# Kernel optimization log

Hardware: AMD Instinct MI355X
Metric: run time of the kernel (lower is better)

Reference implementation:

```python
import jax, jax.numpy as jnp
import numpy as np

PATCH = 3
PAD = 1  # (patchsize-1)//2
PRETRAIN_DIM = 1024
TARGET_DIM = 1024
OUT_H, OUT_W = 224, 224


def _pool_matrix(L_in, L_out):
    """Matrix P s.t. x @ P == torch.adaptive_avg_pool1d(x, L_out)."""
    P = np.zeros((L_in, L_out), dtype=np.float32)
    for i in range(L_out):
        s = (i * L_in) // L_out
        e = -((-(i + 1) * L_in) // L_out)  # ceil
        P[s:e, i] = 1.0 / (e - s)
    return jnp.asarray(P)


def patchify(x):
    """[B,C,H,W] -> [B,H*W,C,3,3], matching Unfold(k=3,s=1,p=1) + reshape/permute."""
    B, C, H, W = x.shape
    xp = jnp.pad(x, ((0, 0), (0, 0), (PAD, PAD), (PAD, PAD)))
    # [B,C,3,3,H,W] with kernel offsets (ki,kj)
    cols = jnp.stack([
        jnp.stack([xp[:, :, i:i + H, j:j + W] for j in range(PATCH)], axis=3)
        for i in range(PATCH)], axis=2)
    return cols.transpose(0, 4, 5, 1, 2, 3).reshape(B, H * W, C, PATCH, PATCH)


def resize_bilinear(x, oh, ow):
    """Bilinear resize of last two dims, align_corners=False (torch semantics)."""
    H, W = x.shape[-2], x.shape[-1]

    def idx(L, O):
        src = (jnp.arange(O, dtype=jnp.float32) + 0.5) * (L / O) - 0.5
        src = jnp.clip(src, 0.0, L - 1)
        i0 = jnp.floor(src).astype(jnp.int32)
        i1 = jnp.minimum(i0 + 1, L - 1)
        return i0, i1, src - i0

    r0, r1, wr = idx(H, oh)
    c0, c1, wc = idx(W, ow)
    xr = x[..., r0, :] * (1.0 - wr)[:, None] + x[..., r1, :] * wr[:, None]
    return xr[..., c0] * (1.0 - wc) + xr[..., c1] * wc


def setup_inputs() -> dict:
    key = jax.random.key(0)
    k1, k2, k3 = jax.random.split(key, 3)
    return {
        "feat1": jax.random.normal(k1, (8, 512, 28, 28), dtype=jnp.float32),
        "feat2": jax.random.normal(k2, (8, 1024, 14, 14), dtype=jnp.float32),
        "memory": jax.random.normal(k3, (20000, 1024), dtype=jnp.float32),
    }


def reference(feat1, feat2, memory):
    B, C1, H1, W1 = feat1.shape
    _, C2, H2, W2 = feat2.shape
    N = H1 * W1  # reference patch grid

    # --- patchify (Unfold k=3 s=1 p=1) ---
    p1 = patchify(feat1)                      # [B, N, C1, 3, 3]
    p2 = patchify(feat2)                      # [B, H2*W2, C2, 3, 3]

    # --- multiscale bilinear resize of layer-2 patch grid to ref grid ---
    g = p2.reshape(B, H2, W2, C2, PATCH, PATCH).transpose(0, 3, 4, 5, 1, 2)  # [B,C2,3,3,H2,W2]
    g = resize_bilinear(g, H1, W1)                                           # [B,C2,3,3,H1,W1]
    p2 = g.transpose(0, 4, 5, 1, 2, 3).reshape(B, N, C2, PATCH, PATCH)

    # --- Preprocessing: adaptive_avg_pool1d over flattened patch -> pretrain dim ---
    f1 = p1.reshape(B * N, C1 * PATCH * PATCH) @ _pool_matrix(C1 * PATCH * PATCH, PRETRAIN_DIM)
    f2 = p2.reshape(B * N, C2 * PATCH * PATCH) @ _pool_matrix(C2 * PATCH * PATCH, PRETRAIN_DIM)

    # --- Aggregator: stack layers, adaptive pool to target dim ---
    stacked = jnp.stack([f1, f2], axis=1).reshape(B * N, 2 * PRETRAIN_DIM)
    feats = stacked @ _pool_matrix(2 * PRETRAIN_DIM, TARGET_DIM)  # [B*N, D]

    # --- kNN memory-bank scoring (k=1): min Euclidean distance ---
    d2 = (jnp.sum(feats * feats, axis=-1, keepdims=True)
          - 2.0 * feats @ memory.T
          + jnp.sum(memory * memory, axis=-1))  # [B*N, M]
    dist = jnp.sqrt(jnp.maximum(d2, 0.0))
    patch_scores = jnp.min(dist, axis=1)       # [B*N]

    # --- unpatch + score + raw segmentation map ---
    ps = patch_scores.reshape(B, N)
    image_scores = jnp.max(ps, axis=1)                           # [B]
    raw_maps = resize_bilinear(ps.reshape(B, H1, W1), OUT_H, OUT_W)  # [B,224,224]
    return image_scores, raw_maps
```

## Files before the change

kernel.cpp:

```cpp
#include <hip/hip_runtime.h>
#include <hip/hip_bf16.h>
#include <math.h>

#define BQ 8
#define C1N 512
#define N1 784
#define C2N 1024
#define M2 196
#define NROWS 6272
#define MEMN 20000
#define MEMNP 20096
#define DIMK 1024
#define NKB 32
#define KTB 4096
#define OUTHW 50176
#define NTILEA 49
#define NTILEB 157
#define NWG (NTILEB * NTILEA)

typedef unsigned char u8;
typedef long long i64v;

typedef __attribute__((ext_vector_type(4))) float f32x4;

static __device__ __forceinline__ unsigned int f2ord(float f) {
  unsigned int b = __float_as_uint(f);
  return (b & 0x80000000u) ? ~b : (b | 0x80000000u);
}
static __device__ __forceinline__ float ord2f(unsigned int u) {
  unsigned int b = (u & 0x80000000u) ? (u ^ 0x80000000u) : ~u;
  return __uint_as_float(b);
}

static __device__ __forceinline__ int pack4_fp8(float a, float b, float c, float d) {
  int lo = __builtin_amdgcn_cvt_pk_fp8_f32(a, b, 0, false);
  return __builtin_amdgcn_cvt_pk_fp8_f32(c, d, lo, true);
}
static __device__ __forceinline__ float sumsq4_fp8(int w) {
  float f0 = __builtin_amdgcn_cvt_f32_fp8(w, 0);
  float f1 = __builtin_amdgcn_cvt_f32_fp8(w, 1);
  float f2 = __builtin_amdgcn_cvt_f32_fp8(w, 2);
  float f3 = __builtin_amdgcn_cvt_f32_fp8(w, 3);
  return f0 * f0 + f1 * f1 + f2 * f2 + f3 * f3;
}

static __device__ __forceinline__ void gload16(const void* g, void* l) {
  __builtin_amdgcn_global_load_lds((const __attribute__((address_space(1))) void*)g,
                                   (__attribute__((address_space(3))) void*)l, 16, 0, 0);
}

static __device__ __forceinline__ size_t tiled_idx(int grow, int k) {
  int tile = grow >> 7, row = grow & 127;
  int kb = k >> 5, c = (k >> 3) & 3, e = k & 7;
  return (((size_t)(tile * NKB + kb) * 4 + c) * 128 + row) * 8 + e;
}

static __device__ __forceinline__ float f1val(const float* __restrict__ x, int b, unsigned L) {
  unsigned h = L % 28u; unsigned t = L / 28u;
  unsigned ki = t % 3u; t /= 3u;
  unsigned c = t % 512u; t /= 512u;
  unsigned w = t % 28u; unsigned kj = t / 28u;
  unsigned y = h + ki - 1u;
  unsigned xx = w + kj - 1u;
  if (y >= 28u || xx >= 28u) return 0.f;
  return x[(((size_t)b * 512u + c) * 28u + y) * 28u + xx];
}
static __device__ __forceinline__ float f2val(const float* __restrict__ x, int b, unsigned L) {
  unsigned h = L % 14u; unsigned t = L / 14u;
  unsigned ki = t % 3u; t /= 3u;
  unsigned c = t % 1024u; t /= 1024u;
  unsigned w = t % 14u; unsigned kj = t / 14u;
  unsigned y = h + ki - 1u;
  unsigned xx = w + kj - 1u;
  if (y >= 14u || xx >= 14u) return 0.f;
  return x[(((size_t)b * 1024u + c) * 14u + y) * 14u + xx];
}

__global__ __launch_bounds__(256) void feat_a_fp8(const float* __restrict__ feat1,
                                                  u8* __restrict__ At) {
  int id = blockIdx.x * 256 + threadIdx.x;
  if (id >= BQ * 64 * N1) return;
  int n = id % N1; int t = id / N1;
  int jc = t % 64; int b = t / 64;
  float v[8];
#pragma unroll
  for (int e = 0; e < 8; ++e) {
    int j = jc * 8 + e;
    unsigned L0 = 9u * (unsigned)(512 * n + j);
    float s = 0.f;
#pragma unroll
    for (int u = 0; u < 9; ++u) s += f1val(feat1, b, L0 + u);
    s += f1val(feat1, b, L0 + 4u);
    v[e] = s * 0.1f;
  }
  int w0 = pack4_fp8(v[0], v[1], v[2], v[3]);
  int w1 = pack4_fp8(v[4], v[5], v[6], v[7]);
  *(int2*)&At[tiled_idx(b * N1 + n, jc * 8)] = make_int2(w0, w1);
}

__global__ __launch_bounds__(256) void feat_b_stage1(const float* __restrict__ feat2,
                                                     float* __restrict__ H2all) {
  int b = blockIdx.x / M2;
  int n2 = blockIdx.x % M2;
  for (int i = threadIdx.x; i < 512; i += 256) {
    unsigned L0 = 18u * (unsigned)(512 * n2 + i);
    float s = 0.f;
#pragma unroll
    for (int u = 0; u < 18; ++u) s += f2val(feat2, b, L0 + u);
    H2all[((size_t)b * M2 + n2) * 512 + i] = s * (1.0f / 18.0f);
  }
}

__global__ __launch_bounds__(256) void feat_b_stage2_fp8(const float* __restrict__ H2all,
                                                         u8* __restrict__ At) {
  int id = blockIdx.x * 256 + threadIdx.x;
  if (id >= BQ * 64 * N1) return;
  int n = id % N1; int t = id / N1;
  int ic = t % 64; int b = t / 64;
  int y = n / 28, x = n % 28;
  float sy = 0.5f * (float)y - 0.25f;
  sy = fminf(fmaxf(sy, 0.f), 13.f);
  int y0 = (int)sy, y1 = min(y0 + 1, 13);
  float wy = sy - (float)y0;
  float sx = 0.5f * (float)x - 0.25f;
  sx = fminf(fmaxf(sx, 0.f), 13.f);
  int x0 = (int)sx, x1 = min(x0 + 1, 13);
  float wx = sx - (float)x0;
  float w00 = (1.f - wy) * (1.f - wx), w10 = wy * (1.f - wx);
  float w01 = (1.f - wy) * wx, w11 = wy * wx;
  const float* h00 = H2all + ((size_t)b * M2 + y0 * 14 + x0) * 512 + ic * 8;
  const float* h10 = H2all + ((size_t)b * M2 + y1 * 14 + x0) * 512 + ic * 8;
  const float* h01 = H2all + ((size_t)b * M2 + y0 * 14 + x1) * 512 + ic * 8;
  const float* h11 = H2all + ((size_t)b * M2 + y1 * 14 + x1) * 512 + ic * 8;
  float v[8];
#pragma unroll
  for (int e = 0; e < 8; ++e)
    v[e] = w00 * h00[e] + w10 * h10[e] + w01 * h01[e] + w11 * h11[e];
  int w0 = pack4_fp8(v[0], v[1], v[2], v[3]);
  int w1 = pack4_fp8(v[4], v[5], v[6], v[7]);
  *(int2*)&At[tiled_idx(b * N1 + n, 512 + ic * 8)] = make_int2(w0, w1);
}

__global__ __launch_bounds__(256) void memconv_fp8(const float* __restrict__ mem,
                                                   u8* __restrict__ Bt) {
  int gid = blockIdx.x * 256 + threadIdx.x;
  if (gid >= NTILEB * NKB * 512) return;
  int tile = gid >> 14;
  int within = gid & 16383;
  int kb = within >> 9;
  int u = within & 511;
  int c = u >> 7, row = u & 127;
  int n = tile * 128 + row;
  int k0 = kb * 32 + c * 8;
  int w0 = 0, w1 = 0;
  if (n < MEMN) {
    const float* src = mem + (size_t)n * DIMK + k0;
    float4 a = *(const float4*)src;
    float4 b = *(const float4*)(src + 4);
    w0 = pack4_fp8(a.x, a.y, a.z, a.w);
    w1 = pack4_fp8(b.x, b.y, b.z, b.w);
  }
  *(int2*)&Bt[(size_t)gid * 8] = make_int2(w0, w1);
}

__global__ __launch_bounds__(256) void fnorm_fp8(const u8* __restrict__ At,
                                                 float* __restrict__ fnorm) {
  int row = blockIdx.x * 4 + (threadIdx.x >> 6);
  int lane = threadIdx.x & 63;
  float s = 0.f;
#pragma unroll
  for (int qq = 0; qq < 2; ++qq) {
    int kc = lane * 2 + qq;
    int2 d = *(const int2*)&At[tiled_idx(row, kc * 8)];
    s += sumsq4_fp8(d.x);
    s += sumsq4_fp8(d.y);
  }
#pragma unroll
  for (int off = 32; off; off >>= 1) s += __shfl_down(s, off, 64);
  if (lane == 0) fnorm[row] = s;
}

__global__ __launch_bounds__(256) void mnorm_fp8(const float* __restrict__ memory,
                                                 float* __restrict__ mnorm) {
  __shared__ float red[4];
  const int row = blockIdx.x;
  const float4 v = *(const float4*)&memory[(size_t)row * DIMK + threadIdx.x * 4];
  int p0 = __builtin_amdgcn_cvt_pk_fp8_f32(v.x, v.y, 0, false);
  int p1 = __builtin_amdgcn_cvt_pk_fp8_f32(v.z, v.w, 0, false);
  float q0 = __builtin_amdgcn_cvt_f32_fp8(p0, 0);
  float q1 = __builtin_amdgcn_cvt_f32_fp8(p0, 1);
  float q2 = __builtin_amdgcn_cvt_f32_fp8(p1, 0);
  float q3 = __builtin_amdgcn_cvt_f32_fp8(p1, 1);
  float s = q0 * q0 + q1 * q1 + q2 * q2 + q3 * q3;
#pragma unroll
  for (int off = 32; off; off >>= 1) s += __shfl_down(s, off, 64);
  if ((threadIdx.x & 63) == 0) red[threadIdx.x >> 6] = s;
  __syncthreads();
  if (threadIdx.x == 0) mnorm[row] = red[0] + red[1] + red[2] + red[3];
}

__global__ __launch_bounds__(256, 4) void dist_min_mfma(const u8* __restrict__ At,
                                                        const u8* __restrict__ Bt,
                                                        const float* __restrict__ mnorm,
                                                        unsigned int* __restrict__ minu) {
  __shared__ __align__(16) u8 LAs[3][4096];
  __shared__ __align__(16) u8 LBs[3][4096];
  const int t = threadIdx.x;
  const int wave = t >> 6, lane = t & 63;

  int lid = blockIdx.x;
  const int q = NWG / 8, r = NWG % 8;
  int xcd = lid & 7, pos = lid >> 3;
  int wgid = (xcd < r ? xcd * (q + 1) : r * (q + 1) + (xcd - r) * q) + pos;
  int g = wgid / (NTILEB * 7), rem = wgid % (NTILEB * 7);
  int bx = rem / 7;
  int by = g * 7 + rem % 7;
  const int row0 = by * 128, col0 = bx * 128;

  f32x4 acc[4][4];
#pragma unroll
  for (int i = 0; i < 4; ++i)
#pragma unroll
    for (int j = 0; j < 4; ++j) acc[i][j] = (f32x4){0.f, 0.f, 0.f, 0.f};

  const int wr = (wave >> 1) * 64, wc = (wave & 1) * 64;
  const int frow = lane & 15, fc = lane >> 4;
  const int aoff = fc * 1024 + (wr + frow) * 8;
  const int boff = fc * 1024 + (wc + frow) * 8;
  const int soff = wave * 1024 + lane * 16;

  const u8* aG = At + (size_t)by * (NKB * KTB) + soff;
  const u8* bG = Bt + (size_t)bx * (NKB * KTB) + soff;

#define STAGE(buf)                            \
  do {                                        \
    gload16(aG, &LAs[buf][wave * 1024]);      \
    gload16(bG, &LBs[buf][wave * 1024]);      \
    aG += KTB; bG += KTB;                     \
  } while (0)

#define COMPUTE(buf)                                                                         \
  do {                                                                                       \
    i64v a[4], b[4];                                                                         \
    _Pragma("unroll") for (int mi = 0; mi < 4; ++mi)                                         \
        a[mi] = *(const i64v*)&LAs[buf][aoff + mi * 128];                                    \
    _Pragma("unroll") for (int ni = 0; ni < 4; ++ni)                                         \
        b[ni] = *(const i64v*)&LBs[buf][boff + ni * 128];                                    \
    __builtin_amdgcn_s_setprio(1);                                                           \
    _Pragma("unroll") for (int mi = 0; mi < 4; ++mi)                                         \
      _Pragma("unroll") for (int ni = 0; ni < 4; ++ni)                                       \
          acc[mi][ni] = __builtin_amdgcn_mfma_f32_16x16x32_fp8_fp8(a[mi], b[ni],             \
                                                                   acc[mi][ni], 0, 0, 0);    \
    __builtin_amdgcn_s_setprio(0);                                                           \
  } while (0)

#define WAITBAR(n)                                        \
  do {                                                    \
    asm volatile("s_waitcnt vmcnt(" #n ")" ::: "memory"); \
    __builtin_amdgcn_s_barrier();                         \
  } while (0)

  STAGE(0);
  STAGE(1);
  WAITBAR(2);

#pragma unroll 1
  for (int i = 0; i < 10; ++i) {
    STAGE(2); COMPUTE(0); WAITBAR(2);
    STAGE(0); COMPUTE(1); WAITBAR(2);
    STAGE(1); COMPUTE(2); WAITBAR(2);
  }
  COMPUTE(0);
  WAITBAR(0);
  COMPUTE(1);
#undef STAGE
#undef COMPUTE
#undef WAITBAR

  float cmn[4];
#pragma unroll
  for (int ni = 0; ni < 4; ++ni) {
    int gn = col0 + wc + ni * 16 + frow;
    cmn[ni] = (gn < MEMN) ? mnorm[gn] : INFINITY;
  }
#pragma unroll
  for (int mi = 0; mi < 4; ++mi) {
#pragma unroll
    for (int rr = 0; rr < 4; ++rr) {
      float v = INFINITY;
#pragma unroll
      for (int ni = 0; ni < 4; ++ni)
        v = fminf(v, fmaf(-2.f, acc[mi][ni][rr], cmn[ni]));
#pragma unroll
      for (int off = 1; off < 16; off <<= 1)
        v = fminf(v, __shfl_xor(v, off, 64));
      if (frow == 0) {
        int grow = row0 + wr + mi * 16 + (lane >> 4) * 4 + rr;
        atomicMin(&minu[grow], f2ord(v));
      }
    }
  }
}


__global__ __launch_bounds__(256) void scores_kernel(const float* __restrict__ fnorm,
                                                     const unsigned int* __restrict__ minu,
                                                     float* __restrict__ scores) {
  int row = blockIdx.x * 256 + threadIdx.x;
  if (row >= NROWS) return;
  float d2 = fnorm[row] + ord2f(minu[row]);
  scores[row] = sqrtf(fmaxf(d2, 0.f));
}

__global__ __launch_bounds__(256) void image_max_kernel(const float* __restrict__ scores,
                                                        float* __restrict__ out) {
  __shared__ float red[4];
  const int b = blockIdx.x;
  float m = -INFINITY;
  for (int n = threadIdx.x; n < N1; n += 256) m = fmaxf(m, scores[b * N1 + n]);
#pragma unroll
  for (int off = 32; off; off >>= 1) m = fmaxf(m, __shfl_down(m, off, 64));
  if ((threadIdx.x & 63) == 0) red[threadIdx.x >> 6] = m;
  __syncthreads();
  if (threadIdx.x == 0) out[b] = fmaxf(fmaxf(red[0], red[1]), fmaxf(red[2], red[3]));
}

__global__ __launch_bounds__(256) void upsample_kernel(const float* __restrict__ scores,
                                                       float* __restrict__ out) {
  int o = blockIdx.x * 256 + threadIdx.x;
  if (o >= BQ * OUTHW) return;
  int b = o / OUTHW, rem = o % OUTHW;
  int oy = rem / 224, ox = rem % 224;
  float sy = ((float)oy + 0.5f) * 0.125f - 0.5f;
  sy = fminf(fmaxf(sy, 0.f), 27.f);
  int y0 = (int)sy, y1 = min(y0 + 1, 27);
  float wy = sy - (float)y0;
  float sx = ((float)ox + 0.5f) * 0.125f - 0.5f;
  sx = fminf(fmaxf(sx, 0.f), 27.f);
  int x0 = (int)sx, x1 = min(x0 + 1, 27);
  float wx = sx - (float)x0;
  const float* s = scores + b * N1;
  float v0 = s[y0 * 28 + x0] * (1.f - wy) + s[y1 * 28 + x0] * wy;
  float v1 = s[y0 * 28 + x1] * (1.f - wy) + s[y1 * 28 + x1] * wy;
  out[BQ + o] = v0 * (1.f - wx) + v1 * wx;
}

extern "C" void kernel_launch(void* const* d_in, const int* in_sizes, int n_in,
                              void* d_out, int out_size, void* d_ws, size_t ws_size,
                              hipStream_t stream) {
  const float* feat1 = (const float*)d_in[0];
  const float* feat2 = (const float*)d_in[1];
  const float* memory = (const float*)d_in[2];
  float* out = (float*)d_out;

  char* ws = (char*)d_ws;
  size_t off = 0;
  auto wsalloc = [&](size_t bytes) {
    void* p = ws + off;
    off += (bytes + 255) & ~(size_t)255;
    return p;
  };

  u8* At = (u8*)wsalloc((size_t)NTILEA * NKB * KTB);
  u8* Bt = (u8*)wsalloc((size_t)NTILEB * NKB * KTB);
  float* mnorm = (float*)wsalloc((size_t)MEMN * 4);
  float* fnorm = (float*)wsalloc((size_t)NROWS * 4);
  unsigned int* minu = (unsigned int*)wsalloc((size_t)NROWS * 4);
  float* scores = (float*)wsalloc((size_t)NROWS * 4);
  float* H2all = (float*)Bt;

  feat_a_fp8<<<(BQ * 64 * N1) / 256, 256, 0, stream>>>(feat1, At);
  feat_b_stage1<<<BQ * M2, 256, 0, stream>>>(feat2, H2all);
  feat_b_stage2_fp8<<<(BQ * 64 * N1) / 256, 256, 0, stream>>>(H2all, At);
  memconv_fp8<<<(NTILEB * NKB * 512) / 256, 256, 0, stream>>>(memory, Bt);
  fnorm_fp8<<<NROWS / 4, 256, 0, stream>>>(At, fnorm);
  mnorm_fp8<<<MEMN, 256, 0, stream>>>(memory, mnorm);
  hipMemsetAsync(minu, 0xFF, (size_t)NROWS * 4, stream);

  dist_min_mfma<<<NWG, 256, 0, stream>>>(At, Bt, mnorm, minu);

  scores_kernel<<<(NROWS + 255) / 256, 256, 0, stream>>>(fnorm, minu, scores);
  image_max_kernel<<<BQ, 256, 0, stream>>>(scores, out);
  upsample_kernel<<<(BQ * OUTHW + 255) / 256, 256, 0, stream>>>(scores, out);
}
```

Baseline: 364.7 us.

## Deepen K tile to 64, pre-transpose and pad features, fuse norm into scores

The GEMM k-tile doubles from 32 to 64 bytes per stage, so each stage loads twice as much data and runs two MFMA sub-steps per barrier. This halves the number of barriers and stage rounds, at the cost of more LDS use and a lower occupancy bound (3 instead of 4). Feature maps are first copied into zero-padded transposed buffers, which removes bounds checks from the patch gather and is meant to make those reads more coalesced, but adds two extra passes over the features. The separate fnorm kernel is folded into the score kernel, and mnorm does one packed fp8 conversion instead of two.

```diff
diff --git a/kernel.cpp b/kernel.cpp
--- a/kernel.cpp
+++ b/kernel.cpp
@@ -11,8 +11,8 @@
 #define MEMN 20000
 #define MEMNP 20096
 #define DIMK 1024
-#define NKB 32
-#define KTB 4096
+#define NKB 16
+#define SLBB 8192
 #define OUTHW 50176
 #define NTILEA 49
 #define NTILEB 157
@@ -20,7 +20,6 @@
 
 typedef unsigned char u8;
 typedef long long i64v;
-
 typedef __attribute__((ext_vector_type(4))) float f32x4;
 
 static __device__ __forceinline__ unsigned int f2ord(float f) {
@@ -51,32 +50,54 @@
 
 static __device__ __forceinline__ size_t tiled_idx(int grow, int k) {
   int tile = grow >> 7, row = grow & 127;
-  int kb = k >> 5, c = (k >> 3) & 3, e = k & 7;
-  return (((size_t)(tile * NKB + kb) * 4 + c) * 128 + row) * 8 + e;
-}
-
-static __device__ __forceinline__ float f1val(const float* __restrict__ x, int b, unsigned L) {
+  int kb = k >> 6, c = (k >> 3) & 7, e = k & 7;
+  return (((size_t)(tile * NKB + kb) * 8 + c) * 128 + row) * 8 + e;
+}
+
+__global__ __launch_bounds__(256) void trans1(const float* __restrict__ x,
+                                              float* __restrict__ xTp) {
+  __shared__ float sm[N1];
+  const float* src = x + (size_t)blockIdx.x * N1;
+  float* dst = xTp + (size_t)blockIdx.x * 960;
+  for (int i = threadIdx.x; i < N1; i += 256) sm[i] = src[i];
+  __syncthreads();
+  for (int o = threadIdx.x; o < 960; o += 256) {
+    int xxs = o >> 5, ys = o & 31;
+    float v = 0.f;
+    if (xxs >= 1 && xxs <= 28 && ys >= 1 && ys <= 28) v = sm[(ys - 1) * 28 + (xxs - 1)];
+    dst[o] = v;
+  }
+}
+__global__ __launch_bounds__(256) void trans2(const float* __restrict__ x,
+                                              float* __restrict__ x2Tp) {
+  __shared__ float sm[M2];
+  const float* src = x + (size_t)blockIdx.x * M2;
+  float* dst = x2Tp + (size_t)blockIdx.x * 256;
+  for (int i = threadIdx.x; i < M2; i += 256) sm[i] = src[i];
+  __syncthreads();
+  int o = threadIdx.x;
+  int xxs = o >> 4, ys = o & 15;
+  float v = 0.f;
+  if (xxs >= 1 && xxs <= 14 && ys >= 1 && ys <= 14) v = sm[(ys - 1) * 14 + (xxs - 1)];
+  dst[o] = v;
+}
+
+static __device__ __forceinline__ float f1valT(const float* __restrict__ xTp, int b, unsigned L) {
   unsigned h = L % 28u; unsigned t = L / 28u;
   unsigned ki = t % 3u; t /= 3u;
   unsigned c = t % 512u; t /= 512u;
   unsigned w = t % 28u; unsigned kj = t / 28u;
-  unsigned y = h + ki - 1u;
-  unsigned xx = w + kj - 1u;
-  if (y >= 28u || xx >= 28u) return 0.f;
-  return x[(((size_t)b * 512u + c) * 28u + y) * 28u + xx];
-}
-static __device__ __forceinline__ float f2val(const float* __restrict__ x, int b, unsigned L) {
+  return xTp[(((size_t)b * 512u + c) * 30u + (w + kj)) * 32u + (h + ki)];
+}
+static __device__ __forceinline__ float f2valT(const float* __restrict__ x2Tp, int b, unsigned L) {
   unsigned h = L % 14u; unsigned t = L / 14u;
   unsigned ki = t % 3u; t /= 3u;
   unsigned c = t % 1024u; t /= 1024u;
   unsigned w = t % 14u; unsigned kj = t / 14u;
-  unsigned y = h + ki - 1u;
-  unsigned xx = w + kj - 1u;
-  if (y >= 14u || xx >= 14u) return 0.f;
-  return x[(((size_t)b * 1024u + c) * 14u + y) * 14u + xx];
-}
-
-__global__ __launch_bounds__(256) void feat_a_fp8(const float* __restrict__ feat1,
+  return x2Tp[(((size_t)b * 1024u + c) << 8) + ((w + kj) << 4) + (h + ki)];
+}
+
+__global__ __launch_bounds__(256) void feat_a_fp8(const float* __restrict__ xTp,
                                                   u8* __restrict__ At) {
   int id = blockIdx.x * 256 + threadIdx.x;
   if (id >= BQ * 64 * N1) return;
@@ -89,8 +110,8 @@
     unsigned L0 = 9u * (unsigned)(512 * n + j);
     float s = 0.f;
 #pragma unroll
-    for (int u = 0; u < 9; ++u) s += f1val(feat1, b, L0 + u);
-    s += f1val(feat1, b, L0 + 4u);
+    for (int u = 0; u < 9; ++u) s += f1valT(xTp, b, L0 + u);
+    s += f1valT(xTp, b, L0 + 4u);
     v[e] = s * 0.1f;
   }
   int w0 = pack4_fp8(v[0], v[1], v[2], v[3]);
@@ -98,7 +119,7 @@
   *(int2*)&At[tiled_idx(b * N1 + n, jc * 8)] = make_int2(w0, w1);
 }
 
-__global__ __launch_bounds__(256) void feat_b_stage1(const float* __restrict__ feat2,
+__global__ __launch_bounds__(256) void feat_b_stage1(const float* __restrict__ x2Tp,
                                                      float* __restrict__ H2all) {
   int b = blockIdx.x / M2;
   int n2 = blockIdx.x % M2;
@@ -106,7 +127,7 @@
     unsigned L0 = 18u * (unsigned)(512 * n2 + i);
     float s = 0.f;
 #pragma unroll
-    for (int u = 0; u < 18; ++u) s += f2val(feat2, b, L0 + u);
+    for (int u = 0; u < 18; ++u) s += f2valT(x2Tp, b, L0 + u);
     H2all[((size_t)b * M2 + n2) * 512 + i] = s * (1.0f / 18.0f);
   }
 }
@@ -144,14 +165,14 @@
 __global__ __launch_bounds__(256) void memconv_fp8(const float* __restrict__ mem,
                                                    u8* __restrict__ Bt) {
   int gid = blockIdx.x * 256 + threadIdx.x;
-  if (gid >= NTILEB * NKB * 512) return;
+  if (gid >= NTILEB * NKB * 1024) return;
   int tile = gid >> 14;
   int within = gid & 16383;
-  int kb = within >> 9;
-  int u = within & 511;
+  int kb = within >> 10;
+  int u = within & 1023;
   int c = u >> 7, row = u & 127;
   int n = tile * 128 + row;
-  int k0 = kb * 32 + c * 8;
+  int k0 = kb * 64 + c * 8;
   int w0 = 0, w1 = 0;
   if (n < MEMN) {
     const float* src = mem + (size_t)n * DIMK + k0;
@@ -163,23 +184,6 @@
   *(int2*)&Bt[(size_t)gid * 8] = make_int2(w0, w1);
 }
 
-__global__ __launch_bounds__(256) void fnorm_fp8(const u8* __restrict__ At,
-                                                 float* __restrict__ fnorm) {
-  int row = blockIdx.x * 4 + (threadIdx.x >> 6);
-  int lane = threadIdx.x & 63;
-  float s = 0.f;
-#pragma unroll
-  for (int qq = 0; qq < 2; ++qq) {
-    int kc = lane * 2 + qq;
-    int2 d = *(const int2*)&At[tiled_idx(row, kc * 8)];
-    s += sumsq4_fp8(d.x);
-    s += sumsq4_fp8(d.y);
-  }
-#pragma unroll
-  for (int off = 32; off; off >>= 1) s += __shfl_down(s, off, 64);
-  if (lane == 0) fnorm[row] = s;
-}
-
 __global__ __launch_bounds__(256) void mnorm_fp8(const float* __restrict__ memory,
                                                  float* __restrict__ mnorm) {
   __shared__ float red[4];
@@ -187,11 +191,8 @@
   const float4 v = *(const float4*)&memory[(size_t)row * DIMK + threadIdx.x * 4];
   int p0 = __builtin_amdgcn_cvt_pk_fp8_f32(v.x, v.y, 0, false);
   int p1 = __builtin_amdgcn_cvt_pk_fp8_f32(v.z, v.w, 0, false);
-  float q0 = __builtin_amdgcn_cvt_f32_fp8(p0, 0);
-  float q1 = __builtin_amdgcn_cvt_f32_fp8(p0, 1);
-  float q2 = __builtin_amdgcn_cvt_f32_fp8(p1, 0);
-  float q3 = __builtin_amdgcn_cvt_f32_fp8(p1, 1);
-  float s = q0 * q0 + q1 * q1 + q2 * q2 + q3 * q3;
+  float s = sumsq4_fp8(__builtin_amdgcn_cvt_pk_fp8_f32(v.z, v.w, p0, true));
+  (void)p1;
 #pragma unroll
   for (int off = 32; off; off >>= 1) s += __shfl_down(s, off, 64);
   if ((threadIdx.x & 63) == 0) red[threadIdx.x >> 6] = s;
@@ -199,12 +200,12 @@
   if (threadIdx.x == 0) mnorm[row] = red[0] + red[1] + red[2] + red[3];
 }
 
-__global__ __launch_bounds__(256, 4) void dist_min_mfma(const u8* __restrict__ At,
+__global__ __launch_bounds__(256, 3) void dist_min_mfma(const u8* __restrict__ At,
                                                         const u8* __restrict__ Bt,
                                                         const float* __restrict__ mnorm,
                                                         unsigned int* __restrict__ minu) {
-  __shared__ __align__(16) u8 LAs[3][4096];
-  __shared__ __align__(16) u8 LBs[3][4096];
+  __shared__ __align__(16) u8 LAs[3][SLBB];
+  __shared__ __align__(16) u8 LBs[3][SLBB];
   const int t = threadIdx.x;
   const int wave = t >> 6, lane = t & 63;
 
@@ -229,29 +230,33 @@
   const int boff = fc * 1024 + (wc + frow) * 8;
   const int soff = wave * 1024 + lane * 16;
 
-  const u8* aG = At + (size_t)by * (NKB * KTB) + soff;
-  const u8* bG = Bt + (size_t)bx * (NKB * KTB) + soff;
-
-#define STAGE(buf)                            \
-  do {                                        \
-    gload16(aG, &LAs[buf][wave * 1024]);      \
-    gload16(bG, &LBs[buf][wave * 1024]);      \
-    aG += KTB; bG += KTB;                     \
+  const u8* aG = At + (size_t)by * (NKB * SLBB) + soff;
+  const u8* bG = Bt + (size_t)bx * (NKB * SLBB) + soff;
+
+#define STAGE(buf)                                  \
+  do {                                              \
+    gload16(aG,        &LAs[buf][wave * 1024]);     \
+    gload16(aG + 4096, &LAs[buf][4096 + wave * 1024]); \
+    gload16(bG,        &LBs[buf][wave * 1024]);     \
+    gload16(bG + 4096, &LBs[buf][4096 + wave * 1024]); \
+    aG += SLBB; bG += SLBB;                         \
   } while (0)
 
 #define COMPUTE(buf)                                                                         \
   do {                                                                                       \
-    i64v a[4], b[4];                                                                         \
-    _Pragma("unroll") for (int mi = 0; mi < 4; ++mi)                                         \
-        a[mi] = *(const i64v*)&LAs[buf][aoff + mi * 128];                                    \
-    _Pragma("unroll") for (int ni = 0; ni < 4; ++ni)                                         \
-        b[ni] = *(const i64v*)&LBs[buf][boff + ni * 128];                                    \
-    __builtin_amdgcn_s_setprio(1);                                                           \
-    _Pragma("unroll") for (int mi = 0; mi < 4; ++mi)                                         \
+    _Pragma("unroll") for (int kk = 0; kk < 2; ++kk) {                                       \
+      i64v a[4], b[4];                                                                       \
+      _Pragma("unroll") for (int mi = 0; mi < 4; ++mi)                                       \
+          a[mi] = *(const i64v*)&LAs[buf][kk * 4096 + aoff + mi * 128];                      \
       _Pragma("unroll") for (int ni = 0; ni < 4; ++ni)                                       \
-          acc[mi][ni] = __builtin_amdgcn_mfma_f32_16x16x32_fp8_fp8(a[mi], b[ni],             \
-                                                                   acc[mi][ni], 0, 0, 0);    \
-    __builtin_amdgcn_s_setprio(0);                                                           \
+          b[ni] = *(const i64v*)&LBs[buf][kk * 4096 + boff + ni * 128];                      \
+      __builtin_amdgcn_s_setprio(1);                                                         \
+      _Pragma("unroll") for (int mi = 0; mi < 4; ++mi)                                       \
+        _Pragma("unroll") for (int ni = 0; ni < 4; ++ni)                                     \
+            acc[mi][ni] = __builtin_amdgcn_mfma_f32_16x16x32_fp8_fp8(a[mi], b[ni],           \
+                                                                     acc[mi][ni], 0, 0, 0);  \
+      __builtin_amdgcn_s_setprio(0);                                                         \
+    }                                                                                        \
   } while (0)
 
 #define WAITBAR(n)                                        \
@@ -262,17 +267,18 @@
 
   STAGE(0);
   STAGE(1);
-  WAITBAR(2);
+  WAITBAR(4);
 
 #pragma unroll 1
-  for (int i = 0; i < 10; ++i) {
-    STAGE(2); COMPUTE(0); WAITBAR(2);
-    STAGE(0); COMPUTE(1); WAITBAR(2);
-    STAGE(1); COMPUTE(2); WAITBAR(2);
-  }
+  for (int i = 0; i < 4; ++i) {
+    STAGE(2); COMPUTE(0); WAITBAR(4);
+    STAGE(0); COMPUTE(1); WAITBAR(4);
+    STAGE(1); COMPUTE(2); WAITBAR(4);
+  }
+  STAGE(2); COMPUTE(0); WAITBAR(4);
+  STAGE(0); COMPUTE(1); WAITBAR(4);
+  COMPUTE(2); WAITBAR(0);
   COMPUTE(0);
-  WAITBAR(0);
-  COMPUTE(1);
 #undef STAGE
 #undef COMPUTE
 #undef WAITBAR
@@ -303,13 +309,21 @@
 }
 
 
-__global__ __launch_bounds__(256) void scores_kernel(const float* __restrict__ fnorm,
-                                                     const unsigned int* __restrict__ minu,
-                                                     float* __restrict__ scores) {
-  int row = blockIdx.x * 256 + threadIdx.x;
-  if (row >= NROWS) return;
-  float d2 = fnorm[row] + ord2f(minu[row]);
-  scores[row] = sqrtf(fmaxf(d2, 0.f));
+__global__ __launch_bounds__(256) void scores_fused(const u8* __restrict__ At,
+                                                    const unsigned int* __restrict__ minu,
+                                                    float* __restrict__ scores) {
+  int row = blockIdx.x * 4 + (threadIdx.x >> 6);
+  int lane = threadIdx.x & 63;
+  float s = 0.f;
+#pragma unroll
+  for (int qq = 0; qq < 2; ++qq) {
+    int2 d = *(const int2*)&At[tiled_idx(row, (lane + qq * 64) * 8)];
+    s += sumsq4_fp8(d.x);
+    s += sumsq4_fp8(d.y);
+  }
+#pragma unroll
+  for (int off = 32; off; off >>= 1) s += __shfl_down(s, off, 64);
+  if (lane == 0) scores[row] = sqrtf(fmaxf(s + ord2f(minu[row]), 0.f));
 }
 
 __global__ __launch_bounds__(256) void image_max_kernel(const float* __restrict__ scores,
@@ -361,25 +375,27 @@
     return p;
   };
 
-  u8* At = (u8*)wsalloc((size_t)NTILEA * NKB * KTB);
-  u8* Bt = (u8*)wsalloc((size_t)NTILEB * NKB * KTB);
+  u8* At = (u8*)wsalloc((size_t)NTILEA * NKB * SLBB);
+  u8* Bt = (u8*)wsalloc((size_t)NTILEB * NKB * SLBB);
+  float* xTp = (float*)wsalloc((size_t)BQ * 512 * 960 * 4);
+  float* x2Tp = (float*)wsalloc((size_t)BQ * 1024 * 256 * 4);
   float* mnorm = (float*)wsalloc((size_t)MEMN * 4);
-  float* fnorm = (float*)wsalloc((size_t)NROWS * 4);
   unsigned int* minu = (unsigned int*)wsalloc((size_t)NROWS * 4);
   float* scores = (float*)wsalloc((size_t)NROWS * 4);
   float* H2all = (float*)Bt;
 
-  feat_a_fp8<<<(BQ * 64 * N1) / 256, 256, 0, stream>>>(feat1, At);
-  feat_b_stage1<<<BQ * M2, 256, 0, stream>>>(feat2, H2all);
+  trans1<<<BQ * C1N, 256, 0, stream>>>(feat1, xTp);
+  trans2<<<BQ * C2N, 256, 0, stream>>>(feat2, x2Tp);
+  feat_a_fp8<<<(BQ * 64 * N1) / 256, 256, 0, stream>>>(xTp, At);
+  feat_b_stage1<<<BQ * M2, 256, 0, stream>>>(x2Tp, H2all);
   feat_b_stage2_fp8<<<(BQ * 64 * N1) / 256, 256, 0, stream>>>(H2all, At);
-  memconv_fp8<<<(NTILEB * NKB * 512) / 256, 256, 0, stream>>>(memory, Bt);
-  fnorm_fp8<<<NROWS / 4, 256, 0, stream>>>(At, fnorm);
+  memconv_fp8<<<(NTILEB * NKB * 1024) / 256, 256, 0, stream>>>(memory, Bt);
   mnorm_fp8<<<MEMN, 256, 0, stream>>>(memory, mnorm);
-  hipMemsetAsync(minu, 0xFF, (size_t)NROWS * 4, stream);
+  (void)hipMemsetAsync(minu, 0xFF, (size_t)NROWS * 4, stream);
 
   dist_min_mfma<<<NWG, 256, 0, stream>>>(At, Bt, mnorm, minu);
 
-  scores_kernel<<<(NROWS + 255) / 256, 256, 0, stream>>>(fnorm, minu, scores);
+  scores_fused<<<NROWS / 4, 256, 0, stream>>>(At, minu, scores);
   image_max_kernel<<<BQ, 256, 0, stream>>>(scores, out);
   upsample_kernel<<<(BQ * OUTHW + 255) / 256, 256, 0, stream>>>(scores, out);
 }
```

Measured after the change: 665.3 us. 1.82x slower.
